# Performance work log

Hardware: AMD Instinct MI355X
Metric: run time of the kernel (lower is better)

## Reference

```python
import jax, jax.numpy as jnp
import numpy as np

DIM = 512
NB = 8
BS = DIM // NB
MODES = (64, 33)
LAM = 0.01
B, H, W = 4, 128, 128


def setup_inputs() -> dict:
    key = jax.random.key(0)
    ks = jax.random.split(key, 10)
    f32 = jnp.float32
    return {
        "x": jax.random.normal(ks[0], (B, DIM, H, W), dtype=f32),
        "w1_real": jax.random.normal(ks[1], (NB, BS, BS), dtype=f32) * 0.02,
        "w1_imag": jax.random.normal(ks[2], (NB, BS, BS), dtype=f32) * 0.02,
        "b1_real": jax.random.normal(ks[3], (NB, BS), dtype=f32) * 0.02,
        "b1_imag": jax.random.normal(ks[4], (NB, BS), dtype=f32) * 0.02,
        "w2_real": jax.random.normal(ks[5], (NB, BS, BS), dtype=f32) * 0.02,
        "w2_imag": jax.random.normal(ks[6], (NB, BS, BS), dtype=f32) * 0.02,
        "b2_real": jax.random.normal(ks[7], (NB, BS), dtype=f32) * 0.02,
        "b2_imag": jax.random.normal(ks[8], (NB, BS), dtype=f32) * 0.02,
        "fuse_w": jax.random.normal(ks[9], (DIM, DIM), dtype=f32) * 0.02,  # 1x1 conv weight
    }


def _complex_linear(zr, zi, wr, wi, br, bi):
    # z: (B,Hf,Wf,nb,bs), W: (nb,bs,bs)
    yr = jnp.einsum("bhwni,nij->bhwnj", zr, wr) - jnp.einsum("bhwni,nij->bhwnj", zi, wi) + br
    yi = jnp.einsum("bhwni,nij->bhwnj", zr, wi) + jnp.einsum("bhwni,nij->bhwnj", zi, wr) + bi
    return yr, yi


def _softshrink(y, lam):
    return jnp.sign(y) * jnp.maximum(jnp.abs(y) - lam, 0.0)


def reference(x, w1_real, w1_imag, b1_real, b1_imag, w2_real, w2_imag, b2_real, b2_imag, fuse_w):
    b, c, h, w = x.shape
    Z = jnp.fft.rfft2(x, axes=(-2, -1), norm="ortho")  # (B,C,Hf,Wf)
    Hf, Wf = Z.shape[-2], Z.shape[-1]
    # (B,C,Hf,Wf) -> (B,Hf,Wf,nb,bs)
    Zr = jnp.transpose(Z.real.reshape(b, NB, BS, Hf, Wf), (0, 3, 4, 1, 2))
    Zi = jnp.transpose(Z.imag.reshape(b, NB, BS, Hf, Wf), (0, 3, 4, 1, 2))

    hr, hi = _complex_linear(Zr, Zi, w1_real, w1_imag, b1_real, b1_imag)
    hr = jax.nn.gelu(hr, approximate=False)
    hi = jax.nn.gelu(hi, approximate=False)
    yr, yi = _complex_linear(hr, hi, w2_real, w2_imag, b2_real, b2_imag)
    yr = _softshrink(yr, LAM)
    yi = _softshrink(yi, LAM)

    m1, m2 = min(MODES[0], Hf), min(MODES[1], Wf)
    mask = jnp.zeros((Hf, Wf), dtype=bool).at[:m1, :m2].set(True)[None, :, :, None, None]
    Zr_out = jnp.where(mask, yr, Zr)
    Zi_out = jnp.where(mask, yi, Zi)

    # (B,Hf,Wf,nb,bs) -> (B,C,Hf,Wf)
    Zr_out = jnp.transpose(Zr_out, (0, 3, 4, 1, 2)).reshape(b, c, Hf, Wf)
    Zi_out = jnp.transpose(Zi_out, (0, 3, 4, 1, 2)).reshape(b, c, Hf, Wf)
    y = jnp.fft.irfft2(Zr_out + 1j * Zi_out, s=(h, w), axes=(-2, -1), norm="ortho")

    y = jnp.einsum("oc,bchw->bohw", fuse_w, y)  # 1x1 conv, no bias
    return x + y
```

## Files before the change

kernel.cpp:

```cpp
#include <hip/hip_runtime.h>
#include <math.h>


#define LAMB 0.01f
#define TWO_PI_OVER_128 0.049087385212340517f

typedef __attribute__((ext_vector_type(8))) short s8bf;
typedef __attribute__((ext_vector_type(8))) unsigned short us8;
typedef __attribute__((ext_vector_type(4))) float f32x4;
typedef __attribute__((ext_vector_type(8))) _Float16 f16x8;

static __device__ __forceinline__ float gelu_exact(float v) {
    return 0.5f * v * (1.0f + erff(v * 0.7071067811865475f));
}
static __device__ __forceinline__ float softshrink01(float v) {
    float a = fabsf(v) - LAMB;
    a = a > 0.0f ? a : 0.0f;
    return v >= 0.0f ? a : -a;
}
static __device__ __forceinline__ unsigned short f2bf(float f) {
    union { float f; unsigned int u; } v; v.f = f;
    unsigned int r = v.u + 0x7FFFu + ((v.u >> 16) & 1u);
    return (unsigned short)(r >> 16);
}

__global__ __launch_bounds__(256) void k_tw(_Float16* __restrict__ tw) {
    const int idx = blockIdx.x * 256 + threadIdx.x;
    {
        const int h = idx >> 6, r = idx & 63;
        float ss, sc;
        sincosf((float)((h * r) & 127) * TWO_PI_OVER_128, &ss, &sc);
        tw[idx]         = (_Float16)sc;
        tw[8192 + idx]  = (_Float16)ss;
        tw[16384 + idx] = (_Float16)(-ss);
        const float wk = (r == 0) ? 0.5f : 1.0f;
        const float pv = (r <= 32) ? wk * sc * 0.015625f : 0.f;
        const float qv = (r <= 32) ? -wk * ss * 0.015625f : 0.f;
        tw[24576 + idx] = (_Float16)pv;
        tw[32768 + idx] = (_Float16)qv;
    }
    if (idx < 6144) {
        const int k = idx >> 7, w = idx & 127;
        float ss, sc;
        sincosf((float)((w * k) & 127) * TWO_PI_OVER_128, &ss, &sc);
        tw[40960 + idx] = (_Float16)(sc * 0.0078125f);
        tw[47104 + idx] = (_Float16)(-ss * 0.0078125f);
    }
    {
        const int r = idx >> 7, h = idx & 127;
        float ss, sc;
        sincosf((float)((r * h) & 127) * TWO_PI_OVER_128, &ss, &sc);
        tw[53248 + idx] = (_Float16)sc;
        tw[61440 + idx] = (_Float16)ss;
        tw[69632 + idx] = (_Float16)(-ss);
    }
}

__global__ __launch_bounds__(256) void k_fwdm(const float* __restrict__ x,
                                              const _Float16* __restrict__ tw,
                                              float2* __restrict__ zm) {
    __shared__ _Float16 Xs[16384];
    const int bc   = blockIdx.x;
    const int tid  = threadIdx.x;
    const int lane = tid & 63;
    const int wv   = tid >> 6;
    const int m15  = lane & 15;
    const int quad = lane >> 4;

    const _Float16* FWr  = tw + 40960;
    const _Float16* FWi  = tw + 47104;
    const _Float16* FHc  = tw + 53248;
    const _Float16* FHs  = tw + 61440;
    const _Float16* FHsn = tw + 69632;

    const float* xim = x + (size_t)bc * 16384;
    for (int t = tid; t < 2048; t += 256) {
        const int h  = t >> 4;
        const int w0 = (t & 15) * 8;
        float4 a = *(const float4*)&xim[h * 128 + w0];
        float4 b = *(const float4*)&xim[h * 128 + w0 + 4];
        f16x8 v;
        v[0] = (_Float16)a.x; v[1] = (_Float16)a.y;
        v[2] = (_Float16)a.z; v[3] = (_Float16)a.w;
        v[4] = (_Float16)b.x; v[5] = (_Float16)b.y;
        v[6] = (_Float16)b.z; v[7] = (_Float16)b.w;
        *(f16x8*)&Xs[(h * 128 + w0) ^ ((h & 7) << 3)] = v;
    }
    __syncthreads();

    f32x4 yR[2][3], yI[2][3];
    #pragma unroll
    for (int i = 0; i < 2; ++i)
        #pragma unroll
        for (int j = 0; j < 3; ++j) {
            yR[i][j] = (f32x4){0.f, 0.f, 0.f, 0.f};
            yI[i][j] = (f32x4){0.f, 0.f, 0.f, 0.f};
        }
    #pragma unroll
    for (int ks = 0; ks < 4; ++ks) {
        const int ko = ks * 32 + quad * 8;
        f16x8 af[2];
        #pragma unroll
        for (int mt = 0; mt < 2; ++mt) {
            const int h = (wv * 2 + mt) * 16 + m15;
            af[mt] = *(const f16x8*)&Xs[(h * 128 + ko) ^ ((h & 7) << 3)];
        }
        #pragma unroll
        for (int nt = 0; nt < 3; ++nt) {
            const int n = nt * 16 + m15;
            f16x8 br = *(const f16x8*)&FWr[n * 128 + ko];
            f16x8 bi = *(const f16x8*)&FWi[n * 128 + ko];
            #pragma unroll
            for (int mt = 0; mt < 2; ++mt) {
                yR[mt][nt] = __builtin_amdgcn_mfma_f32_16x16x32_f16(af[mt], br, yR[mt][nt], 0, 0, 0);
                yI[mt][nt] = __builtin_amdgcn_mfma_f32_16x16x32_f16(af[mt], bi, yI[mt][nt], 0, 0, 0);
            }
        }
    }
    __syncthreads();

    #pragma unroll
    for (int mt = 0; mt < 2; ++mt)
        #pragma unroll
        for (int nt = 0; nt < 3; ++nt)
            #pragma unroll
            for (int r = 0; r < 4; ++r) {
                const int h = (wv * 2 + mt) * 16 + quad * 4 + r;
                const int k = nt * 16 + m15;
                const int si = (k * 128 + h) ^ ((k & 7) << 3);
                Xs[si]        = (_Float16)yR[mt][nt][r];
                Xs[8192 + si] = (_Float16)yI[mt][nt][r];
            }
    __syncthreads();

    f32x4 zR[3], zI[3];
    #pragma unroll
    for (int j = 0; j < 3; ++j) {
        zR[j] = (f32x4){0.f, 0.f, 0.f, 0.f};
        zI[j] = (f32x4){0.f, 0.f, 0.f, 0.f};
    }
    const int rr = wv * 16 + m15;
    #pragma unroll
    for (int ks = 0; ks < 4; ++ks) {
        const int ko = ks * 32 + quad * 8;
        f16x8 ac  = *(const f16x8*)&FHc[rr * 128 + ko];
        f16x8 as2 = *(const f16x8*)&FHs[rr * 128 + ko];
        f16x8 asn = *(const f16x8*)&FHsn[rr * 128 + ko];
        #pragma unroll
        for (int nt = 0; nt < 3; ++nt) {
            const int n  = nt * 16 + m15;
            const int si = (n * 128 + ko) ^ ((n & 7) << 3);
            f16x8 br = *(const f16x8*)&Xs[si];
            f16x8 bi = *(const f16x8*)&Xs[8192 + si];
            zR[nt] = __builtin_amdgcn_mfma_f32_16x16x32_f16(ac,  br, zR[nt], 0, 0, 0);
            zR[nt] = __builtin_amdgcn_mfma_f32_16x16x32_f16(as2, bi, zR[nt], 0, 0, 0);
            zI[nt] = __builtin_amdgcn_mfma_f32_16x16x32_f16(ac,  bi, zI[nt], 0, 0, 0);
            zI[nt] = __builtin_amdgcn_mfma_f32_16x16x32_f16(asn, br, zI[nt], 0, 0, 0);
        }
    }

    float2* zrow = zm + (size_t)bc * 2112;
    #pragma unroll
    for (int nt = 0; nt < 3; ++nt) {
        const int k = nt * 16 + m15;
        if (k < 33) {
            #pragma unroll
            for (int r = 0; r < 4; ++r) {
                const int rw = wv * 16 + quad * 4 + r;
                zrow[rw * 33 + k] = make_float2(zR[nt][r], zI[nt][r]);
            }
        }
    }
}

__global__ __launch_bounds__(256) void k_mlp(const float* __restrict__ w1r_g,
                                             const float* __restrict__ w1i_g,
                                             const float* __restrict__ b1r_g,
                                             const float* __restrict__ b1i_g,
                                             const float* __restrict__ w2r_g,
                                             const float* __restrict__ w2i_g,
                                             const float* __restrict__ b2r_g,
                                             const float* __restrict__ b2i_g,
                                             float2* __restrict__ zm) {
    __shared__ _Float16 S[32768];
    const int p0  = blockIdx.x * 64;
    const int nb  = blockIdx.y;
    const int b   = blockIdx.z;
    const int tid = threadIdx.x;
    const int lane = tid & 63;
    const int wv   = tid >> 6;
    const int m15  = lane & 15;
    const int quad = lane >> 4;

    {
        const int j  = tid & 63;
        const int i0 = (tid >> 6) * 16;
        const int swz = (j & 7) << 3;
        #pragma unroll
        for (int tbl = 0; tbl < 4; ++tbl) {
            const float* src = (tbl == 0) ? w1r_g : (tbl == 1) ? w1i_g
                             : (tbl == 2) ? w2r_g : w2i_g;
            src += nb * 4096;
            f16x8 v0, v1, n0, n1;
            #pragma unroll
            for (int ii = 0; ii < 8; ++ii) {
                float a = src[(i0 + ii) * 64 + j];
                float c = src[(i0 + 8 + ii) * 64 + j];
                v0[ii] = (_Float16)a; n0[ii] = (_Float16)(-a);
                v1[ii] = (_Float16)c; n1[ii] = (_Float16)(-c);
            }
            const int base = (tbl == 0) ? 0 : (tbl == 1) ? 4096
                           : (tbl == 2) ? 12288 : 16384;
            *(f16x8*)&S[base + ((j * 64 + i0) ^ swz)]     = v0;
            *(f16x8*)&S[base + ((j * 64 + i0 + 8) ^ swz)] = v1;
            if (tbl == 1) {
                *(f16x8*)&S[8192 + ((j * 64 + i0) ^ swz)]     = n0;
                *(f16x8*)&S[8192 + ((j * 64 + i0 + 8) ^ swz)] = n1;
            } else if (tbl == 3) {
                *(f16x8*)&S[20480 + ((j * 64 + i0) ^ swz)]     = n0;
                *(f16x8*)&S[20480 + ((j * 64 + i0 + 8) ^ swz)] = n1;
            }
        }
    }

    const float2* zb = zm + (size_t)(b * 512 + nb * 64) * 2112;
    const int p = p0 + wv * 16 + m15;
    f16x8 azr[2], azi[2];
    #pragma unroll
    for (int ks = 0; ks < 2; ++ks) {
        #pragma unroll
        for (int jj = 0; jj < 8; ++jj) {
            float2 z = zb[(size_t)(ks * 32 + quad * 8 + jj) * 2112 + p];
            azr[ks][jj] = (_Float16)z.x;
            azi[ks][jj] = (_Float16)z.y;
        }
    }
    __syncthreads();

    f32x4 hr[4], hi[4];
    #pragma unroll
    for (int nt = 0; nt < 4; ++nt) {
        hr[nt] = (f32x4){0.f, 0.f, 0.f, 0.f};
        hi[nt] = (f32x4){0.f, 0.f, 0.f, 0.f};
    }
    #pragma unroll
    for (int ks = 0; ks < 2; ++ks) {
        #pragma unroll
        for (int nt = 0; nt < 4; ++nt) {
            const int n  = nt * 16 + m15;
            const int sb = (n * 64 + ks * 32 + quad * 8) ^ ((n & 7) << 3);
            f16x8 bwr = *(const f16x8*)&S[sb];
            f16x8 bwi = *(const f16x8*)&S[4096 + sb];
            f16x8 bwn = *(const f16x8*)&S[8192 + sb];
            hr[nt] = __builtin_amdgcn_mfma_f32_16x16x32_f16(azr[ks], bwr, hr[nt], 0, 0, 0);
            hr[nt] = __builtin_amdgcn_mfma_f32_16x16x32_f16(azi[ks], bwn, hr[nt], 0, 0, 0);
            hi[nt] = __builtin_amdgcn_mfma_f32_16x16x32_f16(azr[ks], bwi, hi[nt], 0, 0, 0);
            hi[nt] = __builtin_amdgcn_mfma_f32_16x16x32_f16(azi[ks], bwr, hi[nt], 0, 0, 0);
        }
    }

    #pragma unroll
    for (int nt = 0; nt < 4; ++nt) {
        const int jj = nt * 16 + m15;
        const float br = b1r_g[nb * 64 + jj];
        const float bi = b1i_g[nb * 64 + jj];
        #pragma unroll
        for (int r = 0; r < 4; ++r) {
            const int m  = wv * 16 + quad * 4 + r;
            const int si = (m * 64 + jj) ^ ((m & 7) << 3);
            S[24576 + si] = (_Float16)gelu_exact(hr[nt][r] + br);
            S[28672 + si] = (_Float16)gelu_exact(hi[nt][r] + bi);
        }
    }
    __syncthreads();

    f16x8 ahr[2], ahi[2];
    #pragma unroll
    for (int ks = 0; ks < 2; ++ks) {
        const int m  = wv * 16 + m15;
        const int sa = (m * 64 + ks * 32 + quad * 8) ^ ((m & 7) << 3);
        ahr[ks] = *(const f16x8*)&S[24576 + sa];
        ahi[ks] = *(const f16x8*)&S[28672 + sa];
    }

    f32x4 yr[4], yi[4];
    #pragma unroll
    for (int nt = 0; nt < 4; ++nt) {
        yr[nt] = (f32x4){0.f, 0.f, 0.f, 0.f};
        yi[nt] = (f32x4){0.f, 0.f, 0.f, 0.f};
    }
    #pragma unroll
    for (int ks = 0; ks < 2; ++ks) {
        #pragma unroll
        for (int nt = 0; nt < 4; ++nt) {
            const int n  = nt * 16 + m15;
            const int sb = (n * 64 + ks * 32 + quad * 8) ^ ((n & 7) << 3);
            f16x8 bwr = *(const f16x8*)&S[12288 + sb];
            f16x8 bwi = *(const f16x8*)&S[16384 + sb];
            f16x8 bwn = *(const f16x8*)&S[20480 + sb];
            yr[nt] = __builtin_amdgcn_mfma_f32_16x16x32_f16(ahr[ks], bwr, yr[nt], 0, 0, 0);
            yr[nt] = __builtin_amdgcn_mfma_f32_16x16x32_f16(ahi[ks], bwn, yr[nt], 0, 0, 0);
            yi[nt] = __builtin_amdgcn_mfma_f32_16x16x32_f16(ahr[ks], bwi, yi[nt], 0, 0, 0);
            yi[nt] = __builtin_amdgcn_mfma_f32_16x16x32_f16(ahi[ks], bwr, yi[nt], 0, 0, 0);
        }
    }

    float2* zw = zm + (size_t)(b * 512 + nb * 64) * 2112;
    #pragma unroll
    for (int nt = 0; nt < 4; ++nt) {
        const int jj = nt * 16 + m15;
        const float br = b2r_g[nb * 64 + jj];
        const float bi = b2i_g[nb * 64 + jj];
        #pragma unroll
        for (int r = 0; r < 4; ++r) {
            const int pp = p0 + wv * 16 + quad * 4 + r;
            const size_t gi = (size_t)jj * 2112 + pp;
            float2 z = zw[gi];
            zw[gi] = make_float2(softshrink01(yr[nt][r] + br) - z.x,
                                 softshrink01(yi[nt][r] + bi) - z.y);
        }
    }
}

__global__ __launch_bounds__(256) void k_inv(const float2* __restrict__ zm,
                                             const float* __restrict__ x,
                                             const _Float16* __restrict__ tw,
                                             unsigned short* __restrict__ yb) {
    __shared__ char SB[33792];
    _Float16* Sh = (_Float16*)SB;
    float*    Sb = (float*)SB;
    const int bc   = blockIdx.x;
    const int tid  = threadIdx.x;
    const int lane = tid & 63;
    const int wv   = tid >> 6;
    const int m15  = lane & 15;
    const int quad = lane >> 4;

    const _Float16* T1c  = tw;
    const _Float16* T1s  = tw + 8192;
    const _Float16* T1sn = tw + 16384;
    const _Float16* Pt   = tw + 24576;
    const _Float16* Qt   = tw + 32768;

    for (int t = tid; t < 768; t += 256)
        *(float4*)&Sh[t * 8] = (float4){0.f, 0.f, 0.f, 0.f};
    __syncthreads();

    const float2* src = zm + (size_t)bc * 2112;
    for (int t = tid; t < 2112; t += 256) {
        int r = t / 33;
        int k = t - r * 33;
        float2 d = src[t];
        int sidx = (k * 64 + r) ^ ((k & 7) << 3);
        Sh[sidx]        = (_Float16)d.x;
        Sh[3072 + sidx] = (_Float16)d.y;
    }
    __syncthreads();

    f32x4 aR[2][3], aI[2][3];
    #pragma unroll
    for (int i = 0; i < 2; ++i)
        #pragma unroll
        for (int j = 0; j < 3; ++j) {
            aR[i][j] = (f32x4){0.f, 0.f, 0.f, 0.f};
            aI[i][j] = (f32x4){0.f, 0.f, 0.f, 0.f};
        }
    #pragma unroll
    for (int ks = 0; ks < 2; ++ks) {
        const int ko = ks * 32 + quad * 8;
        f16x8 ac[2], ass[2], asn[2];
        #pragma unroll
        for (int mt = 0; mt < 2; ++mt) {
            const int m = (wv * 2 + mt) * 16 + m15;
            ac[mt]  = *(const f16x8*)&T1c[m * 64 + ko];
            ass[mt] = *(const f16x8*)&T1s[m * 64 + ko];
            asn[mt] = *(const f16x8*)&T1sn[m * 64 + ko];
        }
        #pragma unroll
        for (int nt = 0; nt < 3; ++nt) {
            const int n  = nt * 16 + m15;
            const int sb = (n * 64 + ko) ^ ((n & 7) << 3);
            f16x8 br = *(const f16x8*)&Sh[sb];
            f16x8 bi = *(const f16x8*)&Sh[3072 + sb];
            #pragma unroll
            for (int mt = 0; mt < 2; ++mt) {
                aR[mt][nt] = __builtin_amdgcn_mfma_f32_16x16x32_f16(ac[mt],  br, aR[mt][nt], 0, 0, 0);
                aR[mt][nt] = __builtin_amdgcn_mfma_f32_16x16x32_f16(asn[mt], bi, aR[mt][nt], 0, 0, 0);
                aI[mt][nt] = __builtin_amdgcn_mfma_f32_16x16x32_f16(ac[mt],  bi, aI[mt][nt], 0, 0, 0);
                aI[mt][nt] = __builtin_amdgcn_mfma_f32_16x16x32_f16(ass[mt], br, aI[mt][nt], 0, 0, 0);
            }
        }
    }
    __syncthreads();

    for (int t = tid; t < 2048; t += 256)
        *(float4*)&Sh[t * 8] = (float4){0.f, 0.f, 0.f, 0.f};
    __syncthreads();

    #pragma unroll
    for (int mt = 0; mt < 2; ++mt)
        #pragma unroll
        for (int nt = 0; nt < 3; ++nt)
            #pragma unroll
            for (int r = 0; r < 4; ++r) {
                const int h  = (wv * 2 + mt) * 16 + quad * 4 + r;
                const int k  = nt * 16 + m15;
                const int si = (h * 64 + k) ^ ((h & 7) << 3);
                Sh[si]        = (_Float16)aR[mt][nt][r];
                Sh[8192 + si] = (_Float16)aI[mt][nt][r];
            }
    __syncthreads();

    f16x8 atr[2][2], ati[2][2];
    #pragma unroll
    for (int mt = 0; mt < 2; ++mt) {
        const int hh = (wv * 2 + mt) * 16 + m15;
        #pragma unroll
        for (int ks = 0; ks < 2; ++ks) {
            const int sa = (hh * 64 + ks * 32 + quad * 8) ^ ((hh & 7) << 3);
            atr[mt][ks] = *(const f16x8*)&Sh[sa];
            ati[mt][ks] = *(const f16x8*)&Sh[8192 + sa];
        }
    }
    __syncthreads();

    const size_t base = (size_t)bc * 16384;
    #pragma unroll
    for (int mt = 0; mt < 2; ++mt) {
        f32x4 acc[8];
        #pragma unroll
        for (int nt = 0; nt < 8; ++nt) acc[nt] = (f32x4){0.f, 0.f, 0.f, 0.f};
        #pragma unroll
        for (int ks = 0; ks < 2; ++ks) {
            #pragma unroll
            for (int nt = 0; nt < 8; ++nt) {
                const int go = (nt * 16 + m15) * 64 + ks * 32 + quad * 8;
                f16x8 bp = *(const f16x8*)&Pt[go];
                f16x8 bq = *(const f16x8*)&Qt[go];
                acc[nt] = __builtin_amdgcn_mfma_f32_16x16x32_f16(atr[mt][ks], bp, acc[nt], 0, 0, 0);
                acc[nt] = __builtin_amdgcn_mfma_f32_16x16x32_f16(ati[mt][ks], bq, acc[nt], 0, 0, 0);
            }
        }
        #pragma unroll
        for (int nt = 0; nt < 8; ++nt)
            #pragma unroll
            for (int r = 0; r < 4; ++r)
                Sb[(wv * 16 + quad * 4 + r) * 132 + nt * 16 + m15] = acc[nt][r];
        __syncthreads();

        for (int it = 0; it < 4; ++it) {
            const int off = (it * 256 + tid) * 8;
            const int rbl = off >> 7;
            const int col = off & 127;
            const int h   = ((rbl >> 4) * 2 + mt) * 16 + (rbl & 15);
            const size_t gx = base + (size_t)h * 128 + col;
            float4 s0 = *(const float4*)&Sb[rbl * 132 + col];
            float4 s1 = *(const float4*)&Sb[rbl * 132 + col + 4];
            float4 x0 = *(const float4*)&x[gx];
            float4 x1 = *(const float4*)&x[gx + 4];
            us8 o;
            o[0] = f2bf(x0.x + s0.x); o[1] = f2bf(x0.y + s0.y);
            o[2] = f2bf(x0.z + s0.z); o[3] = f2bf(x0.w + s0.w);
            o[4] = f2bf(x1.x + s1.x); o[5] = f2bf(x1.y + s1.y);
            o[6] = f2bf(x1.z + s1.z); o[7] = f2bf(x1.w + s1.w);
            *(us8*)&yb[gx] = o;
        }
        __syncthreads();
    }
}

__global__ __launch_bounds__(256) void k_tr(const unsigned short* __restrict__ yb,
                                            unsigned short* __restrict__ yt) {
    __shared__ float ts[64][65];
    const int p0 = blockIdx.x * 64;
    const int c0 = blockIdx.y * 64;
    const int b  = blockIdx.z;
    const int t  = threadIdx.x;
    const int lane = t & 63;

    const unsigned short* src = yb + (((size_t)(b * 512 + c0 + lane)) << 14) + p0;
    #pragma unroll
    for (int cc = 0; cc < 2; ++cc) {
        int ch = (t >> 6) * 2 + cc;
        us8 v = *(const us8*)&src[ch * 8];
        #pragma unroll
        for (int j = 0; j < 8; ++j)
            ts[ch * 8 + j][lane] = __uint_as_float((unsigned)v[j] << 16);
    }
    __syncthreads();

    const int pr   = t >> 2;
    const int coff = (t & 3) * 16;
    us8 o0v, o1v;
    #pragma unroll
    for (int i = 0; i < 8; ++i) o0v[i] = f2bf(ts[pr][coff + i]);
    #pragma unroll
    for (int i = 0; i < 8; ++i) o1v[i] = f2bf(ts[pr][coff + 8 + i]);
    unsigned short* dst = yt + ((size_t)(b * 16384 + p0 + pr)) * 512 + c0 + coff;
    *(us8*)&dst[0] = o0v;
    *(us8*)&dst[8] = o1v;
}

__global__ __launch_bounds__(256) void k_prep(const float* __restrict__ fw,
                                              unsigned short* __restrict__ fb) {
    int i = (blockIdx.x * 256 + threadIdx.x) * 4;
    float4 v = *(const float4*)&fw[i];
    ushort4 o;
    o.x = f2bf(v.x); o.y = f2bf(v.y); o.z = f2bf(v.z); o.w = f2bf(v.w);
    *(ushort4*)&fb[i] = o;
}

__global__ __launch_bounds__(256) void k_gemm(const unsigned short* __restrict__ fb,
                                              const unsigned short* __restrict__ yt,
                                              const float* __restrict__ x,
                                              float* __restrict__ out) {
    __shared__ short Al[128 * 40];
    __shared__ short Bl[128 * 40];
    const int p0  = blockIdx.x * 128;
    const int o0  = blockIdx.y * 128;
    const int b   = blockIdx.z;
    const int tid = threadIdx.x;
    const int lane = tid & 63;
    const int w    = tid >> 6;
    const int wo = (w >> 1) * 64, wp = (w & 1) * 64;

    f32x4 acc[4][4];
    #pragma unroll
    for (int i = 0; i < 4; ++i)
        #pragma unroll
        for (int j = 0; j < 4; ++j)
            acc[i][j] = (f32x4){0.f, 0.f, 0.f, 0.f};

    const int m15 = lane & 15, quad = lane >> 4;

    for (int kc = 0; kc < 512; kc += 32) {
        __syncthreads();
        #pragma unroll
        for (int cc = 0; cc < 2; ++cc) {
            int ch = tid + cc * 256;
            int r  = ch >> 2;
            int pt = ch & 3;
            *(s8bf*)&Al[r * 40 + pt * 8] =
                *(const s8bf*)&fb[(size_t)(o0 + r) * 512 + kc + pt * 8];
            *(s8bf*)&Bl[r * 40 + pt * 8] =
                *(const s8bf*)&yt[((size_t)(b * 16384 + p0 + r)) * 512 + kc + pt * 8];
        }
        __syncthreads();

        s8bf af[4], bfr[4];
        #pragma unroll
        for (int i = 0; i < 4; ++i) {
            af[i]  = *(const s8bf*)&Al[(wo + i * 16 + m15) * 40 + quad * 8];
            bfr[i] = *(const s8bf*)&Bl[(wp + i * 16 + m15) * 40 + quad * 8];
        }
        #pragma unroll
        for (int mi = 0; mi < 4; ++mi)
            #pragma unroll
            for (int ni = 0; ni < 4; ++ni)
                acc[mi][ni] = __builtin_amdgcn_mfma_f32_16x16x32_bf16(
                    af[mi], bfr[ni], acc[mi][ni], 0, 0, 0);
    }

    #pragma unroll
    for (int mi = 0; mi < 4; ++mi) {
        #pragma unroll
        for (int ni = 0; ni < 4; ++ni) {
            #pragma unroll
            for (int r = 0; r < 4; ++r) {
                int o = o0 + wo + mi * 16 + quad * 4 + r;
                int p = p0 + wp + ni * 16 + m15;
                size_t idx = (((size_t)(b * 512 + o)) << 14) + p;
                out[idx] = x[idx] + acc[mi][ni][r];
            }
        }
    }
}

extern "C" void kernel_launch(void* const* d_in, const int* in_sizes, int n_in,
                              void* d_out, int out_size, void* d_ws, size_t ws_size,
                              hipStream_t stream) {
    const float* x   = (const float*)d_in[0];
    const float* w1r = (const float*)d_in[1];
    const float* w1i = (const float*)d_in[2];
    const float* b1r = (const float*)d_in[3];
    const float* b1i = (const float*)d_in[4];
    const float* w2r = (const float*)d_in[5];
    const float* w2i = (const float*)d_in[6];
    const float* b2r = (const float*)d_in[7];
    const float* b2i = (const float*)d_in[8];
    const float* fw  = (const float*)d_in[9];
    float* out = (float*)d_out;

    char* ws = (char*)d_ws;
    float2* zm          = (float2*)ws;
    unsigned short* ybf = (unsigned short*)(ws + 34603008);
    unsigned short* yt  = (unsigned short*)(ws + 101711872);
    unsigned short* fb  = (unsigned short*)(ws + 34603008);
    _Float16* tw        = (_Float16*)(ws + 168665088);

    k_tw<<<32, 256, 0, stream>>>(tw);
    k_fwdm<<<2048, 256, 0, stream>>>(x, tw, zm);
    k_mlp<<<dim3(33, 8, 4), 256, 0, stream>>>(w1r, w1i, b1r, b1i,
                                              w2r, w2i, b2r, b2i, zm);
    k_inv<<<2048, 256, 0, stream>>>(zm, x, tw, ybf);
    k_tr<<<dim3(256, 8, 4), 256, 0, stream>>>(ybf, yt);
    k_prep<<<256, 256, 0, stream>>>(fw, fb);
    k_gemm<<<dim3(128, 4, 4), 256, 0, stream>>>(fb, yt, x, out);
}
```

Baseline: 527.7 us.

## Double-buffer LDS tiles in fuse GEMM with register prefetch and XOR swizzle

The 1x1-conv GEMM kernel now keeps two LDS buffers per operand. It prefetches the next K-chunk from global memory into registers while the MFMAs on the current chunk run, then writes that chunk to the other buffer and needs only one barrier per iteration. The padded stride-40 layout is replaced by a stride-32 layout with an XOR swizzle to avoid bank conflicts. This doubles LDS use and adds register pressure, which may lower occupancy.

```diff
diff --git a/kernel.cpp b/kernel.cpp
--- a/kernel.cpp
+++ b/kernel.cpp
@@ -514,8 +514,8 @@
                                               const unsigned short* __restrict__ yt,
                                               const float* __restrict__ x,
                                               float* __restrict__ out) {
-    __shared__ short Al[128 * 40];
-    __shared__ short Bl[128 * 40];
+    __shared__ short Al[2][128 * 32];
+    __shared__ short Bl[2][128 * 32];
     const int p0  = blockIdx.x * 128;
     const int o0  = blockIdx.y * 128;
     const int b   = blockIdx.z;
@@ -533,25 +533,43 @@
 
     const int m15 = lane & 15, quad = lane >> 4;
 
-    for (int kc = 0; kc < 512; kc += 32) {
-        __syncthreads();
-        #pragma unroll
-        for (int cc = 0; cc < 2; ++cc) {
-            int ch = tid + cc * 256;
-            int r  = ch >> 2;
-            int pt = ch & 3;
-            *(s8bf*)&Al[r * 40 + pt * 8] =
-                *(const s8bf*)&fb[(size_t)(o0 + r) * 512 + kc + pt * 8];
-            *(s8bf*)&Bl[r * 40 + pt * 8] =
-                *(const s8bf*)&yt[((size_t)(b * 16384 + p0 + r)) * 512 + kc + pt * 8];
-        }
-        __syncthreads();
+    const int r0 = tid >> 2;
+    const int pt = tid & 3;
+    const int sw = (pt ^ (r0 & 3)) * 8;
+    const size_t gA0 = (size_t)(o0 + r0) * 512 + pt * 8;
+    const size_t gA1 = (size_t)(o0 + r0 + 64) * 512 + pt * 8;
+    const size_t gB0 = ((size_t)(b * 16384 + p0 + r0)) * 512 + pt * 8;
+    const size_t gB1 = ((size_t)(b * 16384 + p0 + r0 + 64)) * 512 + pt * 8;
+    const int l0 = r0 * 32 + sw;
+    const int l1 = (r0 + 64) * 32 + sw;
+
+    s8bf ra0, ra1, rb0, rb1;
+
+    ra0 = *(const s8bf*)&fb[gA0];
+    ra1 = *(const s8bf*)&fb[gA1];
+    rb0 = *(const s8bf*)&yt[gB0];
+    rb1 = *(const s8bf*)&yt[gB1];
+    *(s8bf*)&Al[0][l0] = ra0;  *(s8bf*)&Al[0][l1] = ra1;
+    *(s8bf*)&Bl[0][l0] = rb0;  *(s8bf*)&Bl[0][l1] = rb1;
+    __syncthreads();
+
+    int cur = 0;
+    for (int t = 0; t < 16; ++t) {
+        if (t < 15) {
+            const int kc = (t + 1) * 32;
+            ra0 = *(const s8bf*)&fb[gA0 + kc];
+            ra1 = *(const s8bf*)&fb[gA1 + kc];
+            rb0 = *(const s8bf*)&yt[gB0 + kc];
+            rb1 = *(const s8bf*)&yt[gB1 + kc];
+        }
 
         s8bf af[4], bfr[4];
         #pragma unroll
         for (int i = 0; i < 4; ++i) {
-            af[i]  = *(const s8bf*)&Al[(wo + i * 16 + m15) * 40 + quad * 8];
-            bfr[i] = *(const s8bf*)&Bl[(wp + i * 16 + m15) * 40 + quad * 8];
+            const int ra = wo + i * 16 + m15;
+            const int rb = wp + i * 16 + m15;
+            af[i]  = *(const s8bf*)&Al[cur][ra * 32 + ((quad ^ (ra & 3)) * 8)];
+            bfr[i] = *(const s8bf*)&Bl[cur][rb * 32 + ((quad ^ (rb & 3)) * 8)];
         }
         #pragma unroll
         for (int mi = 0; mi < 4; ++mi)
@@ -559,6 +577,14 @@
             for (int ni = 0; ni < 4; ++ni)
                 acc[mi][ni] = __builtin_amdgcn_mfma_f32_16x16x32_bf16(
                     af[mi], bfr[ni], acc[mi][ni], 0, 0, 0);
+
+        if (t < 15) {
+            const int nx = cur ^ 1;
+            *(s8bf*)&Al[nx][l0] = ra0;  *(s8bf*)&Al[nx][l1] = ra1;
+            *(s8bf*)&Bl[nx][l0] = rb0;  *(s8bf*)&Bl[nx][l1] = rb1;
+            __syncthreads();
+            cur = nx;
+        }
     }
 
     #pragma unroll
```

After: 508.4 us. -3.6%, faster.
